# Performance work log

Hardware: AMD Instinct MI355X
Metric: run time of the kernel (lower is better)

## Reference

```python
import jax, jax.numpy as jnp
import numpy as np

NUM_REL = 20000
NUM_EDGES = 640000
DIM_IN = 128
DIM_OUT = 128
NUM_HEAD = 8
DIM_HID = DIM_OUT // NUM_HEAD
NUM_BIN = 10
NEG_SLOPE = 0.2


def leaky_relu(x):
    return jnp.where(x >= 0, x, NEG_SLOPE * x)


def setup_inputs() -> dict:
    key = jax.random.key(0)
    ks = jax.random.split(key, 8)
    emb_rel = jax.random.normal(ks[0], (NUM_REL, DIM_IN), dtype=jnp.float32)
    head = jax.random.randint(ks[1], (NUM_EDGES, 1), 0, NUM_REL)
    tail = jax.random.randint(ks[2], (NUM_EDGES, 1), 0, NUM_REL)
    bins = jax.random.randint(ks[3], (NUM_EDGES, 1), 0, NUM_BIN)
    relation_triplets = jnp.concatenate([head, tail, bins], axis=-1).astype(jnp.int64)
    # xavier-normal-ish init
    attn_proj_w = jax.random.normal(ks[4], (DIM_OUT, 2 * DIM_IN), dtype=jnp.float32) * (2.0 / np.sqrt(2 * DIM_IN + DIM_OUT))
    attn_proj_b = jnp.zeros((DIM_OUT,), dtype=jnp.float32)
    attn_bin = jax.random.normal(ks[5], (NUM_BIN, NUM_HEAD, 1), dtype=jnp.float32) * 0.3
    attn_vec = jax.random.normal(ks[6], (1, NUM_HEAD, DIM_HID), dtype=jnp.float32) * (2.0 / np.sqrt(NUM_HEAD * DIM_HID))
    aggr_proj_w = jax.random.normal(ks[7], (DIM_OUT, DIM_IN), dtype=jnp.float32) * (2.0 / np.sqrt(DIM_IN + DIM_OUT))
    aggr_proj_b = jnp.zeros((DIM_OUT,), dtype=jnp.float32)
    return {"emb_rel": emb_rel, "relation_triplets": relation_triplets,
            "attn_proj_w": attn_proj_w, "attn_proj_b": attn_proj_b,
            "attn_bin": attn_bin, "attn_vec": attn_vec,
            "aggr_proj_w": aggr_proj_w, "aggr_proj_b": aggr_proj_b}


def reference(emb_rel, relation_triplets, attn_proj_w, attn_proj_b, attn_bin, attn_vec, aggr_proj_w, aggr_proj_b):
    num_rel = emb_rel.shape[0]
    head = relation_triplets[..., 0]
    tail = relation_triplets[..., 1]
    bins = relation_triplets[..., 2]
    # edge gather + concat: [E, 2*dim_in]
    concat = jnp.concatenate([emb_rel[head], emb_rel[tail]], axis=-1)
    proj = concat @ attn_proj_w.T + attn_proj_b  # [E, dim_out]
    proj = leaky_relu(proj).reshape(-1, NUM_HEAD, DIM_HID)
    attn_raw = (proj * attn_vec).sum(axis=-1, keepdims=True) + leaky_relu(attn_bin[bins])  # [E,H,1]
    # per-head-relation segment softmax over edges grouped by head index
    seg_max = jax.ops.segment_max(attn_raw, head, num_segments=num_rel)  # [R,H,1]
    attn_val = jnp.exp(attn_raw - seg_max[head])
    seg_sum = jax.ops.segment_sum(attn_val, head, num_segments=num_rel)  # [R,H,1]
    beta = attn_val / (seg_sum[head] + 1e-16)
    msg = (emb_rel[tail] @ aggr_proj_w.T + aggr_proj_b).reshape(-1, NUM_HEAD, DIM_HID)
    out = jax.ops.segment_sum(beta * msg, head, num_segments=num_rel)  # [R,H,Dh]
    return out.reshape(num_rel, -1)
```

## Files before the change

### kernel.cpp

```cpp
#include <hip/hip_runtime.h>
#include <hip/hip_bf16.h>
#include <cstdint>
#include <cstddef>

#define NUM_REL    20000
#define NUM_EDGES  640000
#define DIM        128
#define NUM_HEAD   8
#define DIM_HID    16
#define NUM_BIN    10
#define CAP        128
#define PROJ_BLKS  471
#define SC_BLKS    2500

using u16 = unsigned short;
using u32 = unsigned int;
typedef __attribute__((ext_vector_type(8))) short bf16x8;
typedef __attribute__((ext_vector_type(4))) float f32x4;

__device__ __forceinline__ float b2f(u16 u) { return __uint_as_float(((u32)u) << 16); }
__device__ __forceinline__ float lo2f(u32 u) { return __uint_as_float(u << 16); }
__device__ __forceinline__ float hi2f(u32 u) { return __uint_as_float(u & 0xffff0000u); }
__device__ __forceinline__ float lrelu(float x) { return fmaxf(x, 0.2f * x); }
__device__ __forceinline__ int clampi(int v, int hi) { return v < 0 ? 0 : (v > hi ? hi : v); }
__device__ __forceinline__ float ldf(const void* p, int f32m, int i)
{ return f32m ? ((const float*)p)[i] : b2f(((const u16*)p)[i]); }
__device__ __forceinline__ u16 f2b(float x)
{ u32 u = __float_as_uint(x); u += 0x7fffu + ((u >> 16) & 1u); return (u16)(u >> 16); }
__device__ __forceinline__ u32 pk2(float a, float b)
{ return (u32)f2b(a) | ((u32)f2b(b) << 16); }

__device__ __forceinline__ void detect_flags(const int* __restrict__ trip,
                                             const u16* __restrict__ emb,
                                             int* sF, int tid)
{
    if (tid < 64) {
        bool odd_zero = (trip[2 * tid + 1] == 0) && (trip[2 * tid + 129] == 0);
        unsigned long long m1 = __ballot(odd_zero);
        int ex = (emb[2 * tid] >> 7) & 0xFF;
        bool inr = (ex >= 110) && (ex <= 136);
        unsigned long long m2 = __ballot(inr);
        if (tid == 0) {
            sF[0] = (~m1 == 0ull) ? 1 : 0;
            sF[1] = (__popcll(m2) >= 32) ? 0 : 1;
        }
    }
    __syncthreads();
}

__global__ __launch_bounds__(256) void k_projscatter(
    const void* __restrict__ emb, const int* __restrict__ trip,
    const void* __restrict__ w_attn, const void* __restrict__ w_aggr,
    const void* __restrict__ b_attn, const void* __restrict__ b_aggr,
    float* __restrict__ A, u16* __restrict__ Bb, u16* __restrict__ Mb,
    int* __restrict__ cnt, int* __restrict__ bucket)
{
    __shared__ u16 sA[128 * 128];
    __shared__ u16 sW[128 * 128];
    __shared__ float sBias[128];
    __shared__ int sF[2];

    const int tid = threadIdx.x;
    detect_flags(trip, (const u16*)emb, sF, tid);
    const int is64 = sF[0], f32m = sF[1];

    if (blockIdx.x >= PROJ_BLKS) {
        int e = (blockIdx.x - PROJ_BLKS) * 256 + tid;
        if (e < NUM_EDGES) {
            int h, t, b;
            if (is64) { h = trip[6 * e]; t = trip[6 * e + 2]; b = trip[6 * e + 4]; }
            else      { h = trip[3 * e]; t = trip[3 * e + 1]; b = trip[3 * e + 2]; }
            h = clampi(h, NUM_REL - 1);
            t = clampi(t, NUM_REL - 1);
            b = clampi(b, NUM_BIN - 1);
            int pos = atomicAdd(&cnt[h], 1);
            if (pos < CAP) bucket[h * CAP + pos] = t | (b << 20);
        }
        return;
    }

    const int mt = blockIdx.x / 3, nt = blockIdx.x % 3;
    const int r0 = mt * 128;

    if (tid < 128)
        sBias[tid] = (nt == 0) ? 0.f : ldf((nt == 1) ? b_attn : b_aggr, f32m, tid);

    if (f32m) {
        const float* src = (const float*)emb;
        #pragma unroll
        for (int i = 0; i < 16; ++i) {
            int f = i * 256 + tid;
            int row = f >> 5, pos = f & 31;
            int g = r0 + row;
            float4 x = (g < NUM_REL) ? ((const float4*)(src + (size_t)g * DIM))[pos]
                                     : make_float4(0.f, 0.f, 0.f, 0.f);
            int chunk = (pos >> 1) ^ (row & 15);
            *(uint2*)&sA[row * 128 + chunk * 8 + (pos & 1) * 4] =
                make_uint2(pk2(x.x, x.y), pk2(x.z, x.w));
        }
    } else {
        const u16* src = (const u16*)emb;
        #pragma unroll
        for (int i = 0; i < 8; ++i) {
            int f = i * 256 + tid;
            int row = f >> 4, pos = f & 15;
            int g = r0 + row;
            uint4 x = (g < NUM_REL) ? ((const uint4*)(src + (size_t)g * DIM))[pos]
                                    : make_uint4(0, 0, 0, 0);
            int chunk = pos ^ (row & 15);
            *(uint4*)&sA[row * 128 + chunk * 8] = x;
        }
    }

    {
        const void* wsrc = (nt == 2) ? w_aggr : w_attn;
        const int stride = (nt == 2) ? 128 : 256;
        const int koff   = (nt == 1) ? 128 : 0;
        if (f32m) {
            const float* src = (const float*)wsrc;
            #pragma unroll
            for (int i = 0; i < 16; ++i) {
                int f = i * 256 + tid;
                int row = f >> 5, pos = f & 31;
                float4 x = ((const float4*)(src + (size_t)row * stride + koff))[pos];
                int chunk = (pos >> 1) ^ (row & 15);
                *(uint2*)&sW[row * 128 + chunk * 8 + (pos & 1) * 4] =
                    make_uint2(pk2(x.x, x.y), pk2(x.z, x.w));
            }
        } else {
            const u16* src = (const u16*)wsrc;
            #pragma unroll
            for (int i = 0; i < 8; ++i) {
                int f = i * 256 + tid;
                int row = f >> 4, pos = f & 15;
                uint4 x = ((const uint4*)(src + (size_t)row * stride + koff))[pos];
                int chunk = pos ^ (row & 15);
                *(uint4*)&sW[row * 128 + chunk * 8] = x;
            }
        }
    }
    __syncthreads();

    const int lane = tid & 63, wid = tid >> 6;
    const int wm = (wid >> 1) * 64, wn = (wid & 1) * 64;
    const int ln15 = lane & 15, q = lane >> 4;

    f32x4 acc[4][4] = {};
    #pragma unroll
    for (int kk = 0; kk < 4; ++kk) {
        const int cbase = kk * 4 + q;
        bf16x8 a[4], b[4];
        #pragma unroll
        for (int mi = 0; mi < 4; ++mi) {
            int m = wm + mi * 16 + ln15;
            int c = cbase ^ ln15;
            a[mi] = *(const bf16x8*)&sA[m * 128 + c * 8];
        }
        #pragma unroll
        for (int ni = 0; ni < 4; ++ni) {
            int n = wn + ni * 16 + ln15;
            int c = cbase ^ ln15;
            b[ni] = *(const bf16x8*)&sW[n * 128 + c * 8];
        }
        #pragma unroll
        for (int mi = 0; mi < 4; ++mi)
            #pragma unroll
            for (int ni = 0; ni < 4; ++ni)
                acc[mi][ni] = __builtin_amdgcn_mfma_f32_16x16x32_bf16(
                    a[mi], b[ni], acc[mi][ni], 0, 0, 0);
    }

    #pragma unroll
    for (int mi = 0; mi < 4; ++mi) {
        #pragma unroll
        for (int reg = 0; reg < 4; ++reg) {
            int g = r0 + wm + mi * 16 + q * 4 + reg;
            if (g < NUM_REL) {
                #pragma unroll
                for (int ni = 0; ni < 4; ++ni) {
                    int c = wn + ni * 16 + ln15;
                    float v = acc[mi][ni][reg] + sBias[c];
                    if (nt == 0) {
                        A[(size_t)g * DIM + c] = v;
                    } else if (nt == 1) {
                        int hd = c >> 4, d = c & 15;
                        int pos = ((d >> 3) << 6) + hd * 8 + (d & 7);
                        Bb[(size_t)g * DIM + pos] = f2b(v);
                    } else {
                        Mb[(size_t)g * DIM + c] = f2b(v);
                    }
                }
            }
        }
    }
}

__global__ __launch_bounds__(256, 6) void k_segment(
    const float* __restrict__ A, const u16* __restrict__ Bb,
    const u16* __restrict__ Mb, const void* __restrict__ attn_bin,
    const void* __restrict__ attn_vec, const int* __restrict__ cnt,
    const int* __restrict__ bucket, const int* __restrict__ trip,
    const void* __restrict__ emb, void* __restrict__ out)
{
    __shared__ float sAr[4][DIM];
    __shared__ float sVec[DIM];
    __shared__ float sBin[NUM_BIN * NUM_HEAD];
    __shared__ int sF[2];

    const int tid  = threadIdx.x;
    detect_flags(trip, (const u16*)emb, sF, tid);
    const int f32m = sF[1];

    const int wid  = tid >> 6, lane = tid & 63;
    const int r = blockIdx.x * 4 + wid;
    int nE = cnt[r]; if (nE > CAP) nE = CAP;
    const int* __restrict__ bk = bucket + r * CAP;

    {
        const float2* ap = (const float2*)(A + (size_t)r * DIM);
        float2 a2 = ap[lane];
        sAr[wid][2 * lane] = a2.x; sAr[wid][2 * lane + 1] = a2.y;
    }
    if (tid < DIM) sVec[tid] = ldf(attn_vec, f32m, tid);
    else if (tid < DIM + NUM_BIN * NUM_HEAD)
        sBin[tid - DIM] = lrelu(ldf(attn_bin, f32m, tid - DIM));
    __syncthreads();

    if (nE == 0) {
        if (f32m) ((float2*)out)[(size_t)r * 64 + lane] = make_float2(0.f, 0.f);
        else      ((u32*)out)[(size_t)r * 64 + lane] = 0;
        return;
    }

    const int el = lane >> 3, hd = lane & 7;
    const int ah = lane >> 3;

    float av[16], vv[16];
    {
        const float4* pA = (const float4*)(&sAr[wid][hd * DIM_HID]);
        const float4* pV = (const float4*)(&sVec[hd * DIM_HID]);
        #pragma unroll
        for (int i = 0; i < 4; ++i) {
            float4 a4 = pA[i], v4 = pV[i];
            av[4*i+0]=a4.x; av[4*i+1]=a4.y; av[4*i+2]=a4.z; av[4*i+3]=a4.w;
            vv[4*i+0]=v4.x; vv[4*i+1]=v4.y; vv[4*i+2]=v4.z; vv[4*i+3]=v4.w;
        }
    }

    float l = 0.f, accx = 0.f, accy = 0.f;

    for (int base = 0; base < nE; base += 8) {
        int e = base + el;
        bool act = e < nE;
        int tb = 0;
        if (act) tb = bk[e];
        int t = tb & 0xFFFFF;
        float p = 0.f;
        if (act) {
            int b = (tb >> 20) & 0xF;
            const uint4* Bt = (const uint4*)(Bb + (size_t)t * DIM);
            uint4 q0 = Bt[hd];
            uint4 q1 = Bt[8 + hd];
            float s = sBin[b * NUM_HEAD + hd];
            s += lrelu(av[0]  + lo2f(q0.x)) * vv[0];
            s += lrelu(av[1]  + hi2f(q0.x)) * vv[1];
            s += lrelu(av[2]  + lo2f(q0.y)) * vv[2];
            s += lrelu(av[3]  + hi2f(q0.y)) * vv[3];
            s += lrelu(av[4]  + lo2f(q0.z)) * vv[4];
            s += lrelu(av[5]  + hi2f(q0.z)) * vv[5];
            s += lrelu(av[6]  + lo2f(q0.w)) * vv[6];
            s += lrelu(av[7]  + hi2f(q0.w)) * vv[7];
            s += lrelu(av[8]  + lo2f(q1.x)) * vv[8];
            s += lrelu(av[9]  + hi2f(q1.x)) * vv[9];
            s += lrelu(av[10] + lo2f(q1.y)) * vv[10];
            s += lrelu(av[11] + hi2f(q1.y)) * vv[11];
            s += lrelu(av[12] + lo2f(q1.z)) * vv[12];
            s += lrelu(av[13] + hi2f(q1.z)) * vv[13];
            s += lrelu(av[14] + lo2f(q1.w)) * vv[14];
            s += lrelu(av[15] + hi2f(q1.w)) * vv[15];
            s = fminf(fmaxf(s, -60.f), 60.f);
            p = __expf(s);
        }
        l += p;

        int lim = nE - base; if (lim > 8) lim = 8;
        #pragma unroll
        for (int k = 0; k < 8; ++k) {
            if (k < lim) {
                float v = __shfl(p, k * 8 + ah);
                int tk  = __shfl(t, k * 8);
                u32 mm = *(const u32*)(Mb + (size_t)tk * DIM + 2 * lane);
                accx += v * lo2f(mm);
                accy += v * hi2f(mm);
            }
        }
    }

    float lt = l + __shfl_xor(l, 8);
    lt += __shfl_xor(lt, 16);
    lt += __shfl_xor(lt, 32);
    float lA = __shfl(lt, ah);
    float inv = 1.0f / (lA + 1e-16f);
    float o0 = accx * inv, o1 = accy * inv;
    if (f32m) {
        ((float2*)out)[(size_t)r * 64 + lane] = make_float2(o0, o1);
    } else {
        u32 pk = (u32)f2b(o0) | ((u32)f2b(o1) << 16);
        ((u32*)out)[(size_t)r * 64 + lane] = pk;
    }
}

extern "C" void kernel_launch(void* const* d_in, const int* in_sizes, int n_in,
                              void* d_out, int out_size, void* d_ws, size_t ws_size,
                              hipStream_t stream)
{
    (void)in_sizes; (void)n_in; (void)out_size; (void)ws_size;
    const void* emb      = d_in[0];
    const int*  trip     = (const int*)d_in[1];
    const void* w_attn   = d_in[2];
    const void* b_attn   = d_in[3];
    const void* attn_bin = d_in[4];
    const void* attn_vec = d_in[5];
    const void* w_aggr   = d_in[6];
    const void* b_aggr   = d_in[7];

    char* p = (char*)d_ws;
    float* A      = (float*)p; p += (size_t)NUM_REL * DIM * 4;
    u16*   Bb     = (u16*)p;   p += (size_t)NUM_REL * DIM * 2;
    u16*   Mb     = (u16*)p;   p += (size_t)NUM_REL * DIM * 2;
    int*   bucket = (int*)p;   p += (size_t)NUM_REL * CAP * 4;
    int*   cnt    = (int*)p;   p += (size_t)NUM_REL * 4;

    hipMemsetAsync(cnt, 0, NUM_REL * sizeof(int), stream);
    k_projscatter<<<PROJ_BLKS + SC_BLKS, 256, 0, stream>>>(
        emb, trip, w_attn, w_aggr, b_attn, b_aggr, A, Bb, Mb, cnt, bucket);
    k_segment<<<NUM_REL / 4, 256, 0, stream>>>(A, Bb, Mb, attn_bin, attn_vec,
                                               cnt, bucket, trip, emb, d_out);
}
```

Baseline: 201.7 us.

## Load GEMM A operands directly from global and simplify B projection layout

The projection kernel no longer stages the embedding tile in shared memory. Each lane instead loads its bf16x8 A fragments straight from global memory (converting from f32 when needed), which halves the kernel's LDS footprint and may allow more resident blocks. The B projection is now stored in natural head-contiguous order, and the segment kernel reads two adjacent uint4s per head instead of two strided ones. The cost is uncoalesced, redundant global reads of A across the warps that share rows.

```diff
diff --git a/kernel.cpp b/kernel.cpp
--- a/kernel.cpp
+++ b/kernel.cpp
@@ -55,7 +55,6 @@
     float* __restrict__ A, u16* __restrict__ Bb, u16* __restrict__ Mb,
     int* __restrict__ cnt, int* __restrict__ bucket)
 {
-    __shared__ u16 sA[128 * 128];
     __shared__ u16 sW[128 * 128];
     __shared__ float sBias[128];
     __shared__ int sF[2];
@@ -84,33 +83,6 @@
 
     if (tid < 128)
         sBias[tid] = (nt == 0) ? 0.f : ldf((nt == 1) ? b_attn : b_aggr, f32m, tid);
-
-    if (f32m) {
-        const float* src = (const float*)emb;
-        #pragma unroll
-        for (int i = 0; i < 16; ++i) {
-            int f = i * 256 + tid;
-            int row = f >> 5, pos = f & 31;
-            int g = r0 + row;
-            float4 x = (g < NUM_REL) ? ((const float4*)(src + (size_t)g * DIM))[pos]
-                                     : make_float4(0.f, 0.f, 0.f, 0.f);
-            int chunk = (pos >> 1) ^ (row & 15);
-            *(uint2*)&sA[row * 128 + chunk * 8 + (pos & 1) * 4] =
-                make_uint2(pk2(x.x, x.y), pk2(x.z, x.w));
-        }
-    } else {
-        const u16* src = (const u16*)emb;
-        #pragma unroll
-        for (int i = 0; i < 8; ++i) {
-            int f = i * 256 + tid;
-            int row = f >> 4, pos = f & 15;
-            int g = r0 + row;
-            uint4 x = (g < NUM_REL) ? ((const uint4*)(src + (size_t)g * DIM))[pos]
-                                    : make_uint4(0, 0, 0, 0);
-            int chunk = pos ^ (row & 15);
-            *(uint4*)&sA[row * 128 + chunk * 8] = x;
-        }
-    }
 
     {
         const void* wsrc = (nt == 2) ? w_aggr : w_attn;
@@ -145,16 +117,32 @@
     const int wm = (wid >> 1) * 64, wn = (wid & 1) * 64;
     const int ln15 = lane & 15, q = lane >> 4;
 
+    int arow[4];
+    #pragma unroll
+    for (int mi = 0; mi < 4; ++mi) {
+        int g = r0 + wm + mi * 16 + ln15;
+        arow[mi] = (g < NUM_REL) ? g : (NUM_REL - 1);
+    }
+
     f32x4 acc[4][4] = {};
     #pragma unroll
     for (int kk = 0; kk < 4; ++kk) {
         const int cbase = kk * 4 + q;
+        const int kc = cbase * 8;
         bf16x8 a[4], b[4];
         #pragma unroll
         for (int mi = 0; mi < 4; ++mi) {
-            int m = wm + mi * 16 + ln15;
-            int c = cbase ^ ln15;
-            a[mi] = *(const bf16x8*)&sA[m * 128 + c * 8];
+            if (f32m) {
+                const float* er = (const float*)emb + (size_t)arow[mi] * DIM + kc;
+                float4 x0 = *(const float4*)er;
+                float4 x1 = *(const float4*)(er + 4);
+                union { bf16x8 v; u32 u[4]; } cv;
+                cv.u[0] = pk2(x0.x, x0.y); cv.u[1] = pk2(x0.z, x0.w);
+                cv.u[2] = pk2(x1.x, x1.y); cv.u[3] = pk2(x1.z, x1.w);
+                a[mi] = cv.v;
+            } else {
+                a[mi] = *(const bf16x8*)((const u16*)emb + (size_t)arow[mi] * DIM + kc);
+            }
         }
         #pragma unroll
         for (int ni = 0; ni < 4; ++ni) {
@@ -180,15 +168,10 @@
                 for (int ni = 0; ni < 4; ++ni) {
                     int c = wn + ni * 16 + ln15;
                     float v = acc[mi][ni][reg] + sBias[c];
-                    if (nt == 0) {
-                        A[(size_t)g * DIM + c] = v;
-                    } else if (nt == 1) {
-                        int hd = c >> 4, d = c & 15;
-                        int pos = ((d >> 3) << 6) + hd * 8 + (d & 7);
-                        Bb[(size_t)g * DIM + pos] = f2b(v);
-                    } else {
-                        Mb[(size_t)g * DIM + c] = f2b(v);
-                    }
+                    size_t o = (size_t)g * DIM + c;
+                    if (nt == 0)      A[o]  = v;
+                    else if (nt == 1) Bb[o] = f2b(v);
+                    else              Mb[o] = f2b(v);
                 }
             }
         }
@@ -258,9 +241,8 @@
         float p = 0.f;
         if (act) {
             int b = (tb >> 20) & 0xF;
-            const uint4* Bt = (const uint4*)(Bb + (size_t)t * DIM);
-            uint4 q0 = Bt[hd];
-            uint4 q1 = Bt[8 + hd];
+            const uint4* Bt = (const uint4*)(Bb + (size_t)t * DIM) + hd * 2;
+            uint4 q0 = Bt[0], q1 = Bt[1];
             float s = sBin[b * NUM_HEAD + hd];
             s += lrelu(av[0]  + lo2f(q0.x)) * vv[0];
             s += lrelu(av[1]  + hi2f(q0.x)) * vv[1];
```

Measured after the change: 183.7 us. -9.0%, faster.
